# Kernel optimization log

Measured on AMD Instinct MI355X. Metric: run time of the kernel, lower is better.

## Reference

```python
import jax, jax.numpy as jnp
import numpy as np

N = 10000   # num nodes
E = 640000  # num edges
D_IN, D_HID, D_OUT = 128, 256, 128


def _cheb_layer(x, src, dst, dis, W0, W1, b):
    """PyG ChebConv with K=2, sym norm, lambda_max=2.0 (no edge weights):
    out = x @ W0 + (L_hat x) @ W1 + b, with L_hat = -D^{-1/2} A D^{-1/2}."""
    norm = -(dis[src] * dis[dst])                       # [E]
    msg = norm[:, None] * x[src]                        # [E, d]
    tx1 = jax.ops.segment_sum(msg, dst, num_segments=N)  # [N, d]
    return x @ W0 + tx1 @ W1 + b


def setup_inputs() -> dict:
    key = jax.random.key(0)
    ks = jax.random.split(key, 10)

    def glorot(k, fan_in, fan_out):
        s = jnp.sqrt(6.0 / (fan_in + fan_out))
        return jax.random.uniform(k, (fan_in, fan_out), jnp.float32, -s, s)

    x = jax.random.normal(ks[0], (N, D_IN), jnp.float32)
    edge_index = jax.random.randint(ks[1], (2, E), 0, N, jnp.int64)
    edge_type = jax.random.randint(ks[2], (E,), 0, 5, jnp.int64)
    return {
        "x": x,
        "edge_index": edge_index,
        "edge_type": edge_type,
        "W01": glorot(ks[3], D_IN, D_HID),
        "W11": glorot(ks[4], D_IN, D_HID),
        "b1": jnp.zeros((D_HID,), jnp.float32),
        "W02": glorot(ks[5], D_HID, D_HID),
        "W12": glorot(ks[6], D_HID, D_HID),
        "b2": jnp.zeros((D_HID,), jnp.float32),
        "W03": glorot(ks[7], D_HID, D_OUT),
        "W13": glorot(ks[8], D_HID, D_OUT),
        "b3": jnp.zeros((D_OUT,), jnp.float32),
    }


def reference(x, edge_index, edge_type, W01, W11, b1, W02, W12, b2, W03, W13, b3):
    # edge_type is unused by ChebConv (matches the original forward signature).
    src, dst = edge_index[0], edge_index[1]
    deg = jax.ops.segment_sum(jnp.ones((E,), x.dtype), src, num_segments=N)
    dis = jnp.where(deg > 0, jax.lax.rsqrt(jnp.maximum(deg, 1.0)), 0.0)
    # eval mode: dropout(p=0.4) is identity
    h = jax.nn.relu(_cheb_layer(x, src, dst, dis, W01, W11, b1))
    h = jax.nn.relu(_cheb_layer(h, src, dst, dis, W02, W12, b2))
    return _cheb_layer(h, src, dst, dis, W03, W13, b3)
```

## Files before the change

### kernel.cpp

```cpp
#include <hip/hip_runtime.h>

#define D_IN 128
#define D_HID 256
#define D_OUT 128
#define NBIN 10240
#define HB 256

typedef __attribute__((ext_vector_type(8))) unsigned short ushort8v;
typedef __attribute__((ext_vector_type(4))) unsigned short ushort4v;
typedef __attribute__((ext_vector_type(8))) short short8v;
typedef __attribute__((ext_vector_type(4))) float f32x4;

__device__ __forceinline__ unsigned short f2bf(float f) {
    unsigned u = __float_as_uint(f);
    unsigned r = (u + 0x7fffu + ((u >> 16) & 1u)) >> 16;
    return (unsigned short)r;
}
__device__ __forceinline__ float bf2f(unsigned short b) {
    return __uint_as_float((unsigned)b << 16);
}


struct WtrArgs {
    const float* W[6];
    unsigned short* T[6];
    int K[6];
    int N[6];
    const float* xin;
    unsigned short* xout;
    int nElem;
};


__global__ __launch_bounds__(256) void k_hist(const int* __restrict__ src, const int* __restrict__ dst,
                                              unsigned short* __restrict__ psrc,
                                              unsigned short* __restrict__ pdst,
                                              int E, int EPB, WtrArgs wa) {
    __shared__ int h[NBIN];
    int b = blockIdx.x, t = threadIdx.x;
    if (blockIdx.y == 2) {
        const int starts[7] = {0, 32, 64, 128, 192, 224, 256};
        int m = 0;
        while (b >= starts[m + 1]) ++m;
        int local = b - starts[m];
        int K = wa.K[m], N = wa.N[m];
        int kt = K / 32;
        int k0 = (local % kt) * 32, n0 = (local / kt) * 32;
        float (*tile)[33] = (float(*)[33])h;
        int tx = t & 31, ty = t >> 5;
        const float* W = wa.W[m];
        unsigned short* Wt = wa.T[m];
        for (int i = ty; i < 32; i += 8) tile[i][tx] = W[(size_t)(k0 + i) * N + n0 + tx];
        __syncthreads();
        for (int i = ty; i < 32; i += 8) Wt[(size_t)(n0 + i) * K + k0 + tx] = f2bf(tile[tx][i]);
        int stride = HB * 256 * 4;
        for (int i = (b * 256 + t) * 4; i < wa.nElem; i += stride) {
            float4 v = *reinterpret_cast<const float4*>(&wa.xin[i]);
            ushort4v o;
            o[0] = f2bf(v.x); o[1] = f2bf(v.y); o[2] = f2bf(v.z); o[3] = f2bf(v.w);
            *reinterpret_cast<ushort4v*>(&wa.xout[i]) = o;
        }
        return;
    }
    const int* arr = blockIdx.y ? dst : src;
    unsigned short* outp = blockIdx.y ? pdst : psrc;
    for (int i = t; i < NBIN; i += 256) h[i] = 0;
    __syncthreads();
    int beg = b * EPB, end = beg + EPB; if (end > E) end = E;
    for (int e = beg + t; e < end; e += 256)
        atomicAdd(&h[arr[e]], 1);
    __syncthreads();
    for (int i = t; i < NBIN; i += 256)
        outp[(size_t)b * NBIN + i] = (unsigned short)h[i];
}


__global__ __launch_bounds__(256) void k_colsum(const unsigned short* __restrict__ psrc,
                                                unsigned short* __restrict__ pdst,
                                                float* __restrict__ dis, int* __restrict__ cnt) {
    int bin = blockIdx.x * 256 + threadIdx.x;
    if (bin >= NBIN) return;
    int degs = 0;
    for (int b = 0; b < HB; ++b) degs += psrc[(size_t)b * NBIN + bin];
    int c = 0;
    for (int b = 0; b < HB; ++b) {
        int v = pdst[(size_t)b * NBIN + bin];
        pdst[(size_t)b * NBIN + bin] = (unsigned short)c;
        c += v;
    }
    dis[bin] = degs > 0 ? rsqrtf((float)degs) : 0.f;
    cnt[bin] = c;
}


__global__ void k_scan(const int* __restrict__ cnt, int* __restrict__ off, int n, int E) {
    __shared__ int sums[256];
    int t = threadIdx.x;
    int chunk = (n + 255) / 256;
    int beg = t * chunk;
    int end = beg + chunk; if (end > n) end = n;
    int s = 0;
    for (int i = beg; i < end; ++i) s += cnt[i];
    sums[t] = s;
    __syncthreads();
    if (t == 0) {
        int running = 0;
        for (int i = 0; i < 256; ++i) { int tmp = sums[i]; sums[i] = running; running += tmp; }
        off[n] = E;
    }
    __syncthreads();
    int pre = sums[t];
    for (int i = beg; i < end; ++i) { off[i] = pre; pre += cnt[i]; }
}


__global__ __launch_bounds__(256) void k_scatter2(const int* __restrict__ src, const int* __restrict__ dst,
                                                  const float* __restrict__ dis, const int* __restrict__ off,
                                                  const unsigned short* __restrict__ pfx,
                                                  unsigned* __restrict__ edges, int E, int EPB) {
    __shared__ int lcnt[NBIN];
    int b = blockIdx.x, t = threadIdx.x;
    for (int i = t; i < NBIN; i += 256) lcnt[i] = 0;
    __syncthreads();
    int beg = b * EPB, end = beg + EPB; if (end > E) end = E;
    const unsigned short* pf = pfx + (size_t)b * NBIN;
    for (int e = beg + t; e < end; e += 256) {
        int s = src[e], d = dst[e];
        int r = atomicAdd(&lcnt[d], 1);
        int pos = off[d] + (int)pf[d] + r;
        float nv = -(dis[s] * dis[d]);
        edges[pos] = ((unsigned)s << 16) | (unsigned)f2bf(nv);
    }
}


#define AGG_GATHER(eSet, vSet)                                                        \
    _Pragma("unroll")                                                                 \
    for (int u = 0; u < 8; ++u)                                                       \
        vSet[u] = *reinterpret_cast<const ushort8v*>(&xb[(size_t)(eSet[u] >> 16) * D + cbase]);

#define AGG_ACCUM(eSet, vSet)                                                         \
    _Pragma("unroll")                                                                 \
    for (int u = 0; u < 8; ++u) {                                                     \
        float nv = __uint_as_float(eSet[u] << 16);                                    \
        _Pragma("unroll")                                                             \
        for (int j = 0; j < 8; ++j)                                                   \
            acc[j] += nv * bf2f(vSet[u][j]);                                          \
    }

template<int D, bool STBF, bool STF32, bool ADDB>
__global__ __launch_bounds__(256) void k_agg_bf(const int* __restrict__ off,
                                                const unsigned* __restrict__ edges,
                                                const unsigned short* __restrict__ xb,
                                                unsigned short* __restrict__ outb,
                                                float* __restrict__ outf,
                                                const float* __restrict__ base, int n) {
    const int CHUNK = 128;
    const int TPN = CHUNK / 8;
    const int NPB = 256 / TPN;
    int tid = threadIdx.x;
    int node = blockIdx.x * NPB + tid / TPN;
    if (node >= n) return;
    int cbase = blockIdx.y * CHUNK + (tid % TPN) * 8;
    int i = off[node], end = off[node + 1];
    float acc[8] = {};
    int nb = (end - i) >> 3;

    if (nb > 0) {
        unsigned e0[8], e1[8];
        ushort8v v0[8], v1[8];
        #pragma unroll
        for (int u = 0; u < 8; ++u) e0[u] = edges[i + u];
        AGG_GATHER(e0, v0)
        int b = 1;
        for (; b + 1 < nb; b += 2) {
            int base1 = i + b * 8;
            #pragma unroll
            for (int u = 0; u < 8; ++u) e1[u] = edges[base1 + u];
            AGG_GATHER(e1, v1)
            AGG_ACCUM(e0, v0)
            int base0 = i + (b + 1) * 8;
            #pragma unroll
            for (int u = 0; u < 8; ++u) e0[u] = edges[base0 + u];
            AGG_GATHER(e0, v0)
            AGG_ACCUM(e1, v1)
        }
        if (b < nb) {
            int base1 = i + b * 8;
            #pragma unroll
            for (int u = 0; u < 8; ++u) e1[u] = edges[base1 + u];
            AGG_GATHER(e1, v1)
            AGG_ACCUM(e0, v0)
            AGG_ACCUM(e1, v1)
        } else {
            AGG_ACCUM(e0, v0)
        }
    }
    for (int t = i + nb * 8; t < end; ++t) {
        unsigned e = edges[t];
        float nv = __uint_as_float(e << 16);
        ushort8v v = *reinterpret_cast<const ushort8v*>(&xb[(size_t)(e >> 16) * D + cbase]);
        #pragma unroll
        for (int j = 0; j < 8; ++j)
            acc[j] += nv * bf2f(v[j]);
    }

    if (ADDB) {
        float4 b0 = *reinterpret_cast<const float4*>(&base[(size_t)node * D + cbase]);
        float4 b1 = *reinterpret_cast<const float4*>(&base[(size_t)node * D + cbase + 4]);
        acc[0] += b0.x; acc[1] += b0.y; acc[2] += b0.z; acc[3] += b0.w;
        acc[4] += b1.x; acc[5] += b1.y; acc[6] += b1.z; acc[7] += b1.w;
    }
    if (STBF) {
        ushort8v ob;
        #pragma unroll
        for (int j = 0; j < 8; ++j) ob[j] = f2bf(acc[j]);
        *reinterpret_cast<ushort8v*>(&outb[(size_t)node * D + cbase]) = ob;
    }
    if (STF32) {
        float4 o0, o1;
        o0.x = acc[0]; o0.y = acc[1]; o0.z = acc[2]; o0.w = acc[3];
        o1.x = acc[4]; o1.y = acc[5]; o1.z = acc[6]; o1.w = acc[7];
        *reinterpret_cast<float4*>(&outf[(size_t)node * D + cbase]) = o0;
        *reinterpret_cast<float4*>(&outf[(size_t)node * D + cbase + 4]) = o1;
    }
}


#define LDT 72

template<int K, bool RELU, bool HAS_B2, bool HAS_BIAS, bool ST_BF, bool ST_F32>
__global__ __launch_bounds__(256) void k_gemm_mfma(
        const unsigned short* __restrict__ A1, const unsigned short* __restrict__ W0t,
        const unsigned short* __restrict__ A2, const unsigned short* __restrict__ W1t,
        const float* __restrict__ bias,
        float* __restrict__ C, unsigned short* __restrict__ Cb, int M, int N) {
    __shared__ unsigned short As[64 * LDT];
    __shared__ unsigned short Bs[128 * LDT];
    int tid = threadIdx.x, lane = tid & 63, wave = tid >> 6;
    int wm = wave >> 1, wn = wave & 1;
    int row0 = blockIdx.x * 64, col0 = blockIdx.y * 128;
    f32x4 acc[2][4];
    #pragma unroll
    for (int i = 0; i < 2; ++i)
        #pragma unroll
        for (int j = 0; j < 4; ++j)
            acc[i][j] = (f32x4){0.f, 0.f, 0.f, 0.f};

    int aRow = wm * 32 + (lane & 15);
    int bRow = wn * 64 + (lane & 15);
    int kOff = (lane >> 4) * 8;
    int sr = tid >> 2, sc = (tid & 3) * 8;
    int gra = row0 + sr; if (gra >= M) gra = M - 1;

    const int npass = HAS_B2 ? 2 : 1;
    for (int pass = 0; pass < npass; ++pass) {
        const unsigned short* A = pass ? A2 : A1;
        const unsigned short* W = pass ? W1t : W0t;
        for (int k0 = 0; k0 < K; k0 += 64) {
            #pragma unroll
            for (int h = 0; h < 2; ++h) {
                ushort8v va = *reinterpret_cast<const ushort8v*>(&A[(size_t)gra * K + k0 + sc + h * 32]);
                *reinterpret_cast<ushort8v*>(&As[sr * LDT + sc + h * 32]) = va;
            }
            #pragma unroll
            for (int g = 0; g < 2; ++g)
                #pragma unroll
                for (int h = 0; h < 2; ++h) {
                    int r = sr + g * 64;
                    ushort8v vb = *reinterpret_cast<const ushort8v*>(&W[(size_t)(col0 + r) * K + k0 + sc + h * 32]);
                    *reinterpret_cast<ushort8v*>(&Bs[r * LDT + sc + h * 32]) = vb;
                }
            __syncthreads();
            #pragma unroll
            for (int kk = 0; kk < 2; ++kk) {
                int ko = kOff + kk * 32;
                short8v a[2], bb[4];
                #pragma unroll
                for (int i = 0; i < 2; ++i)
                    a[i] = *reinterpret_cast<const short8v*>(&As[(aRow + i * 16) * LDT + ko]);
                #pragma unroll
                for (int i = 0; i < 4; ++i)
                    bb[i] = *reinterpret_cast<const short8v*>(&Bs[(bRow + i * 16) * LDT + ko]);
                #pragma unroll
                for (int mi = 0; mi < 2; ++mi)
                    #pragma unroll
                    for (int ni = 0; ni < 4; ++ni)
                        acc[mi][ni] = __builtin_amdgcn_mfma_f32_16x16x32_bf16(a[mi], bb[ni], acc[mi][ni], 0, 0, 0);
            }
            __syncthreads();
        }
    }

    int colBase = col0 + wn * 64 + (lane & 15);
    int rowSub = (lane >> 4) * 4;
    #pragma unroll
    for (int mi = 0; mi < 2; ++mi) {
        int rowF = row0 + wm * 32 + mi * 16 + rowSub;
        #pragma unroll
        for (int r = 0; r < 4; ++r) {
            int gr = rowF + r;
            if (gr < M) {
                #pragma unroll
                for (int ni = 0; ni < 4; ++ni) {
                    int gc = colBase + ni * 16;
                    float v = acc[mi][ni][r];
                    if (HAS_BIAS) v += bias[gc];
                    if (RELU)     v = fmaxf(v, 0.f);
                    if (ST_F32)   C[(size_t)gr * N + gc] = v;
                    if (ST_BF)    Cb[(size_t)gr * N + gc] = f2bf(v);
                }
            }
        }
    }
}


template<int K>
__global__ __launch_bounds__(256) void k_gemm_dual(
        const unsigned short* __restrict__ A1, const unsigned short* __restrict__ W03t,
        const unsigned short* __restrict__ W13t, const float* __restrict__ bias,
        float* __restrict__ part, unsigned short* __restrict__ y3b, int M) {
    const int N = 128;
    __shared__ unsigned short As[64 * LDT];
    __shared__ unsigned short Bs[128 * LDT];
    int tid = threadIdx.x, lane = tid & 63, wave = tid >> 6;
    int wm = wave >> 1, wn = wave & 1;
    int row0 = blockIdx.x * 64;
    const unsigned short* W = blockIdx.y ? W13t : W03t;
    f32x4 acc[2][4];
    #pragma unroll
    for (int i = 0; i < 2; ++i)
        #pragma unroll
        for (int j = 0; j < 4; ++j)
            acc[i][j] = (f32x4){0.f, 0.f, 0.f, 0.f};

    int aRow = wm * 32 + (lane & 15);
    int bRow = wn * 64 + (lane & 15);
    int kOff = (lane >> 4) * 8;
    int sr = tid >> 2, sc = (tid & 3) * 8;
    int gra = row0 + sr; if (gra >= M) gra = M - 1;

    for (int k0 = 0; k0 < K; k0 += 64) {
        #pragma unroll
        for (int h = 0; h < 2; ++h) {
            ushort8v va = *reinterpret_cast<const ushort8v*>(&A1[(size_t)gra * K + k0 + sc + h * 32]);
            *reinterpret_cast<ushort8v*>(&As[sr * LDT + sc + h * 32]) = va;
        }
        #pragma unroll
        for (int g = 0; g < 2; ++g)
            #pragma unroll
            for (int h = 0; h < 2; ++h) {
                int r = sr + g * 64;
                ushort8v vb = *reinterpret_cast<const ushort8v*>(&W[(size_t)r * K + k0 + sc + h * 32]);
                *reinterpret_cast<ushort8v*>(&Bs[r * LDT + sc + h * 32]) = vb;
            }
        __syncthreads();
        #pragma unroll
        for (int kk = 0; kk < 2; ++kk) {
            int ko = kOff + kk * 32;
            short8v a[2], bb[4];
            #pragma unroll
            for (int i = 0; i < 2; ++i)
                a[i] = *reinterpret_cast<const short8v*>(&As[(aRow + i * 16) * LDT + ko]);
            #pragma unroll
            for (int i = 0; i < 4; ++i)
                bb[i] = *reinterpret_cast<const short8v*>(&Bs[(bRow + i * 16) * LDT + ko]);
            #pragma unroll
            for (int mi = 0; mi < 2; ++mi)
                #pragma unroll
                for (int ni = 0; ni < 4; ++ni)
                    acc[mi][ni] = __builtin_amdgcn_mfma_f32_16x16x32_bf16(a[mi], bb[ni], acc[mi][ni], 0, 0, 0);
        }
        __syncthreads();
    }

    int colBase = wn * 64 + (lane & 15);
    int rowSub = (lane >> 4) * 4;
    bool isPart = (blockIdx.y == 0);
    #pragma unroll
    for (int mi = 0; mi < 2; ++mi) {
        int rowF = row0 + wm * 32 + mi * 16 + rowSub;
        #pragma unroll
        for (int r = 0; r < 4; ++r) {
            int gr = rowF + r;
            if (gr < M) {
                #pragma unroll
                for (int ni = 0; ni < 4; ++ni) {
                    int gc = colBase + ni * 16;
                    float v = acc[mi][ni][r];
                    if (isPart) part[(size_t)gr * N + gc] = v + bias[gc];
                    else        y3b[(size_t)gr * N + gc] = f2bf(v);
                }
            }
        }
    }
}


extern "C" void kernel_launch(void* const* d_in, const int* in_sizes, int n_in,
                              void* d_out, int out_size, void* d_ws, size_t ws_size,
                              hipStream_t stream) {
    const float* x   = (const float*)d_in[0];
    const int*   ei  = (const int*)d_in[1];
    const float* W01 = (const float*)d_in[3];
    const float* W11 = (const float*)d_in[4];
    const float* b1  = (const float*)d_in[5];
    const float* W02 = (const float*)d_in[6];
    const float* W12 = (const float*)d_in[7];
    const float* b2  = (const float*)d_in[8];
    const float* W03 = (const float*)d_in[9];
    const float* W13 = (const float*)d_in[10];
    const float* b3  = (const float*)d_in[11];
    float* out = (float*)d_out;

    const int n = in_sizes[0] / D_IN;
    const int E = in_sizes[1] / 2;
    const int* src = ei;
    const int* dst = ei + E;
    const int EPB = (E + HB - 1) / HB;

    char* wsb = (char*)d_ws;
    float* dis   = (float*)wsb;                   wsb += NBIN * 4;
    int*   cnt   = (int*)wsb;                     wsb += NBIN * 4;
    int*   off   = (int*)wsb;                     wsb += (NBIN + 16) * 4;
    unsigned short* psrc = (unsigned short*)wsb;  wsb += (size_t)HB * NBIN * 2;
    unsigned short* pdst = (unsigned short*)wsb;  wsb += (size_t)HB * NBIN * 2;
    unsigned* edges = (unsigned*)wsb;             wsb += (size_t)E * 4;
    unsigned short* txb  = (unsigned short*)wsb;  wsb += (size_t)n * D_HID * 2;
    float*          part = (float*)wsb;           wsb += (size_t)n * D_OUT * 4;
    unsigned short* x_bf = (unsigned short*)wsb;  wsb += (size_t)n * D_IN * 2;
    unsigned short* h1_bf = (unsigned short*)wsb; wsb += (size_t)n * D_HID * 2;
    unsigned short* h2_bf = (unsigned short*)wsb; wsb += (size_t)n * D_HID * 2;
    unsigned short* y3_bf = (unsigned short*)wsb; wsb += (size_t)n * D_OUT * 2;
    unsigned short* W01t = (unsigned short*)wsb;  wsb += (size_t)D_IN  * D_HID * 2;
    unsigned short* W11t = (unsigned short*)wsb;  wsb += (size_t)D_IN  * D_HID * 2;
    unsigned short* W02t = (unsigned short*)wsb;  wsb += (size_t)D_HID * D_HID * 2;
    unsigned short* W12t = (unsigned short*)wsb;  wsb += (size_t)D_HID * D_HID * 2;
    unsigned short* W03t = (unsigned short*)wsb;  wsb += (size_t)D_HID * D_OUT * 2;
    unsigned short* W13t = (unsigned short*)wsb;  wsb += (size_t)D_HID * D_OUT * 2;

    const int gmx = (n + 63) / 64;
    const int gax = (n + 15) / 16;

    WtrArgs wa;
    wa.W[0] = W01; wa.T[0] = W01t; wa.K[0] = D_IN;  wa.N[0] = D_HID;
    wa.W[1] = W11; wa.T[1] = W11t; wa.K[1] = D_IN;  wa.N[1] = D_HID;
    wa.W[2] = W02; wa.T[2] = W02t; wa.K[2] = D_HID; wa.N[2] = D_HID;
    wa.W[3] = W12; wa.T[3] = W12t; wa.K[3] = D_HID; wa.N[3] = D_HID;
    wa.W[4] = W03; wa.T[4] = W03t; wa.K[4] = D_HID; wa.N[4] = D_OUT;
    wa.W[5] = W13; wa.T[5] = W13t; wa.K[5] = D_HID; wa.N[5] = D_OUT;
    wa.xin = x; wa.xout = x_bf; wa.nElem = n * D_IN;

    k_hist<<<dim3(HB, 3), 256, 0, stream>>>(src, dst, psrc, pdst, E, EPB, wa);
    k_colsum<<<NBIN / 256, 256, 0, stream>>>(psrc, pdst, dis, cnt);
    k_scan<<<1, 256, 0, stream>>>(cnt, off, n, E);
    k_scatter2<<<HB, 256, 0, stream>>>(src, dst, dis, off, pdst, edges, E, EPB);

    k_agg_bf<D_IN, true, false, false><<<dim3(gax, 1), 256, 0, stream>>>(
        off, edges, x_bf, txb, nullptr, nullptr, n);
    k_gemm_mfma<D_IN, true, true, true, true, false><<<dim3(gmx, D_HID / 128), 256, 0, stream>>>(
        x_bf, W01t, txb, W11t, b1, nullptr, h1_bf, n, D_HID);

    k_agg_bf<D_HID, true, false, false><<<dim3(gax, 2), 256, 0, stream>>>(
        off, edges, h1_bf, txb, nullptr, nullptr, n);
    k_gemm_mfma<D_HID, true, true, true, true, false><<<dim3(gmx, D_HID / 128), 256, 0, stream>>>(
        h1_bf, W02t, txb, W12t, b2, nullptr, h2_bf, n, D_HID);

    k_gemm_dual<D_HID><<<dim3(gmx, 2), 256, 0, stream>>>(
        h2_bf, W03t, W13t, b3, part, y3_bf, n);
    k_agg_bf<D_OUT, false, true, true><<<dim3(gax, 1), 256, 0, stream>>>(
        off, edges, y3_bf, nullptr, out, part, n);
}
```

Measured before the change: 162.8 us.

## Gather neighbor features in FP8 for all three sparse aggregations

Adds FP8 copies of the input features, the layer-1 activations and the layer-3 projected features, written by the producer kernels. The aggregation kernels then gather these instead of bf16, halving the bytes per random neighbor row read. Each thread now covers 16 columns of the full row, so the column-split grid dimension goes away. The cost is FP8 quantization error in the aggregated features plus extra FP8 stores in the producers, which may hurt accuracy.

```diff
diff --git a/kernel.cpp b/kernel.cpp
--- a/kernel.cpp
+++ b/kernel.cpp
@@ -10,6 +10,8 @@
 typedef __attribute__((ext_vector_type(4))) unsigned short ushort4v;
 typedef __attribute__((ext_vector_type(8))) short short8v;
 typedef __attribute__((ext_vector_type(4))) float f32x4;
+typedef __attribute__((ext_vector_type(2))) float f32x2;
+typedef __attribute__((ext_vector_type(4))) unsigned int uint4v;
 
 __device__ __forceinline__ unsigned short f2bf(float f) {
     unsigned u = __float_as_uint(f);
@@ -18,6 +20,14 @@
 }
 __device__ __forceinline__ float bf2f(unsigned short b) {
     return __uint_as_float((unsigned)b << 16);
+}
+__device__ __forceinline__ unsigned pk_f8x4(float a, float b, float c, float d) {
+    int v = __builtin_amdgcn_cvt_pk_fp8_f32(a, b, 0, false);
+    v = __builtin_amdgcn_cvt_pk_fp8_f32(c, d, v, true);
+    return (unsigned)v;
+}
+__device__ __forceinline__ unsigned char f8_1(float a) {
+    return (unsigned char)(__builtin_amdgcn_cvt_pk_fp8_f32(a, a, 0, false) & 0xff);
 }
 
 
@@ -28,6 +38,7 @@
     int N[6];
     const float* xin;
     unsigned short* xout;
+    unsigned char* xoutf8;
     int nElem;
 };
 
@@ -59,6 +70,7 @@
             ushort4v o;
             o[0] = f2bf(v.x); o[1] = f2bf(v.y); o[2] = f2bf(v.z); o[3] = f2bf(v.w);
             *reinterpret_cast<ushort4v*>(&wa.xout[i]) = o;
+            *reinterpret_cast<unsigned*>(&wa.xoutf8[i]) = pk_f8x4(v.x, v.y, v.z, v.w);
         }
         return;
     }
@@ -137,38 +149,54 @@
 #define AGG_GATHER(eSet, vSet)                                                        \
     _Pragma("unroll")                                                                 \
     for (int u = 0; u < 8; ++u)                                                       \
-        vSet[u] = *reinterpret_cast<const ushort8v*>(&xb[(size_t)(eSet[u] >> 16) * D + cbase]);
+        vSet[u] = *reinterpret_cast<const uint4v*>(&xf8[(size_t)(eSet[u] >> 16) * D + cbase]);
 
 #define AGG_ACCUM(eSet, vSet)                                                         \
     _Pragma("unroll")                                                                 \
     for (int u = 0; u < 8; ++u) {                                                     \
         float nv = __uint_as_float(eSet[u] << 16);                                    \
         _Pragma("unroll")                                                             \
-        for (int j = 0; j < 8; ++j)                                                   \
-            acc[j] += nv * bf2f(vSet[u][j]);                                          \
+        for (int d = 0; d < 4; ++d) {                                                 \
+            f32x2 lo = __builtin_amdgcn_cvt_pk_f32_fp8((int)vSet[u][d], false);       \
+            f32x2 hi = __builtin_amdgcn_cvt_pk_f32_fp8((int)vSet[u][d], true);        \
+            acc[4*d+0] += nv * lo[0]; acc[4*d+1] += nv * lo[1];                       \
+            acc[4*d+2] += nv * hi[0]; acc[4*d+3] += nv * hi[1];                       \
+        }                                                                             \
+    }
+
+#define AGG_ONE(e)                                                                    \
+    {                                                                                 \
+        float nv = __uint_as_float((e) << 16);                                        \
+        uint4v v = *reinterpret_cast<const uint4v*>(&xf8[(size_t)((e) >> 16) * D + cbase]); \
+        _Pragma("unroll")                                                             \
+        for (int d = 0; d < 4; ++d) {                                                 \
+            f32x2 lo = __builtin_amdgcn_cvt_pk_f32_fp8((int)v[d], false);             \
+            f32x2 hi = __builtin_amdgcn_cvt_pk_f32_fp8((int)v[d], true);              \
+            acc[4*d+0] += nv * lo[0]; acc[4*d+1] += nv * lo[1];                       \
+            acc[4*d+2] += nv * hi[0]; acc[4*d+3] += nv * hi[1];                       \
+        }                                                                             \
     }
 
 template<int D, bool STBF, bool STF32, bool ADDB>
-__global__ __launch_bounds__(256) void k_agg_bf(const int* __restrict__ off,
+__global__ __launch_bounds__(256) void k_agg_f8(const int* __restrict__ off,
                                                 const unsigned* __restrict__ edges,
-                                                const unsigned short* __restrict__ xb,
+                                                const unsigned char* __restrict__ xf8,
                                                 unsigned short* __restrict__ outb,
                                                 float* __restrict__ outf,
                                                 const float* __restrict__ base, int n) {
-    const int CHUNK = 128;
-    const int TPN = CHUNK / 8;
+    const int TPN = D / 16;
     const int NPB = 256 / TPN;
     int tid = threadIdx.x;
     int node = blockIdx.x * NPB + tid / TPN;
     if (node >= n) return;
-    int cbase = blockIdx.y * CHUNK + (tid % TPN) * 8;
+    int cbase = (tid % TPN) * 16;
     int i = off[node], end = off[node + 1];
-    float acc[8] = {};
+    float acc[16] = {};
     int nb = (end - i) >> 3;
 
     if (nb > 0) {
         unsigned e0[8], e1[8];
-        ushort8v v0[8], v1[8];
+        uint4v v0[8], v1[8];
         #pragma unroll
         for (int u = 0; u < 8; ++u) e0[u] = edges[i + u];
         AGG_GATHER(e0, v0)
@@ -198,43 +226,42 @@
     }
     for (int t = i + nb * 8; t < end; ++t) {
         unsigned e = edges[t];
-        float nv = __uint_as_float(e << 16);
-        ushort8v v = *reinterpret_cast<const ushort8v*>(&xb[(size_t)(e >> 16) * D + cbase]);
-        #pragma unroll
-        for (int j = 0; j < 8; ++j)
-            acc[j] += nv * bf2f(v[j]);
+        AGG_ONE(e)
     }
 
     if (ADDB) {
-        float4 b0 = *reinterpret_cast<const float4*>(&base[(size_t)node * D + cbase]);
-        float4 b1 = *reinterpret_cast<const float4*>(&base[(size_t)node * D + cbase + 4]);
-        acc[0] += b0.x; acc[1] += b0.y; acc[2] += b0.z; acc[3] += b0.w;
-        acc[4] += b1.x; acc[5] += b1.y; acc[6] += b1.z; acc[7] += b1.w;
+        #pragma unroll
+        for (int q = 0; q < 4; ++q) {
+            float4 bq = *reinterpret_cast<const float4*>(&base[(size_t)node * D + cbase + q * 4]);
+            acc[q*4+0] += bq.x; acc[q*4+1] += bq.y; acc[q*4+2] += bq.z; acc[q*4+3] += bq.w;
+        }
     }
     if (STBF) {
-        ushort8v ob;
-        #pragma unroll
-        for (int j = 0; j < 8; ++j) ob[j] = f2bf(acc[j]);
-        *reinterpret_cast<ushort8v*>(&outb[(size_t)node * D + cbase]) = ob;
+        ushort8v ob0, ob1;
+        #pragma unroll
+        for (int j = 0; j < 8; ++j) { ob0[j] = f2bf(acc[j]); ob1[j] = f2bf(acc[8 + j]); }
+        *reinterpret_cast<ushort8v*>(&outb[(size_t)node * D + cbase]) = ob0;
+        *reinterpret_cast<ushort8v*>(&outb[(size_t)node * D + cbase + 8]) = ob1;
     }
     if (STF32) {
-        float4 o0, o1;
-        o0.x = acc[0]; o0.y = acc[1]; o0.z = acc[2]; o0.w = acc[3];
-        o1.x = acc[4]; o1.y = acc[5]; o1.z = acc[6]; o1.w = acc[7];
-        *reinterpret_cast<float4*>(&outf[(size_t)node * D + cbase]) = o0;
-        *reinterpret_cast<float4*>(&outf[(size_t)node * D + cbase + 4]) = o1;
+        #pragma unroll
+        for (int q = 0; q < 4; ++q) {
+            float4 o;
+            o.x = acc[q*4+0]; o.y = acc[q*4+1]; o.z = acc[q*4+2]; o.w = acc[q*4+3];
+            *reinterpret_cast<float4*>(&outf[(size_t)node * D + cbase + q * 4]) = o;
+        }
     }
 }
 
 
 #define LDT 72
 
-template<int K, bool RELU, bool HAS_B2, bool HAS_BIAS, bool ST_BF, bool ST_F32>
+template<int K, bool RELU, bool HAS_B2, bool HAS_BIAS, bool ST_BF, bool ST_F8>
 __global__ __launch_bounds__(256) void k_gemm_mfma(
         const unsigned short* __restrict__ A1, const unsigned short* __restrict__ W0t,
         const unsigned short* __restrict__ A2, const unsigned short* __restrict__ W1t,
         const float* __restrict__ bias,
-        float* __restrict__ C, unsigned short* __restrict__ Cb, int M, int N) {
+        unsigned short* __restrict__ Cb, unsigned char* __restrict__ Cf8, int M, int N) {
     __shared__ unsigned short As[64 * LDT];
     __shared__ unsigned short Bs[128 * LDT];
     int tid = threadIdx.x, lane = tid & 63, wave = tid >> 6;
@@ -307,8 +334,8 @@
                     float v = acc[mi][ni][r];
                     if (HAS_BIAS) v += bias[gc];
                     if (RELU)     v = fmaxf(v, 0.f);
-                    if (ST_F32)   C[(size_t)gr * N + gc] = v;
                     if (ST_BF)    Cb[(size_t)gr * N + gc] = f2bf(v);
+                    if (ST_F8)    Cf8[(size_t)gr * N + gc] = f8_1(v);
                 }
             }
         }
@@ -320,7 +347,7 @@
 __global__ __launch_bounds__(256) void k_gemm_dual(
         const unsigned short* __restrict__ A1, const unsigned short* __restrict__ W03t,
         const unsigned short* __restrict__ W13t, const float* __restrict__ bias,
-        float* __restrict__ part, unsigned short* __restrict__ y3b, int M) {
+        float* __restrict__ part, unsigned char* __restrict__ y3f8, int M) {
     const int N = 128;
     __shared__ unsigned short As[64 * LDT];
     __shared__ unsigned short Bs[128 * LDT];
@@ -390,7 +417,7 @@
                     int gc = colBase + ni * 16;
                     float v = acc[mi][ni][r];
                     if (isPart) part[(size_t)gr * N + gc] = v + bias[gc];
-                    else        y3b[(size_t)gr * N + gc] = f2bf(v);
+                    else        y3f8[(size_t)gr * N + gc] = f8_1(v);
                 }
             }
         }
@@ -432,7 +459,10 @@
     unsigned short* x_bf = (unsigned short*)wsb;  wsb += (size_t)n * D_IN * 2;
     unsigned short* h1_bf = (unsigned short*)wsb; wsb += (size_t)n * D_HID * 2;
     unsigned short* h2_bf = (unsigned short*)wsb; wsb += (size_t)n * D_HID * 2;
-    unsigned short* y3_bf = (unsigned short*)wsb; wsb += (size_t)n * D_OUT * 2;
+    unsigned char* x_f8  = (unsigned char*)wsb;   wsb += (size_t)n * D_IN;
+    unsigned char* h1_f8 = (unsigned char*)wsb;   wsb += (size_t)n * D_HID;
+    unsigned char* y3_f8 = (unsigned char*)wsb;   wsb += (size_t)n * D_OUT;
+    wsb = (char*)(((size_t)wsb + 255) & ~(size_t)255);
     unsigned short* W01t = (unsigned short*)wsb;  wsb += (size_t)D_IN  * D_HID * 2;
     unsigned short* W11t = (unsigned short*)wsb;  wsb += (size_t)D_IN  * D_HID * 2;
     unsigned short* W02t = (unsigned short*)wsb;  wsb += (size_t)D_HID * D_HID * 2;
@@ -441,7 +471,8 @@
     unsigned short* W13t = (unsigned short*)wsb;  wsb += (size_t)D_HID * D_OUT * 2;
 
     const int gmx = (n + 63) / 64;
-    const int gax = (n + 15) / 16;
+    const int ga128 = (n + 31) / 32;
+    const int ga256 = (n + 15) / 16;
 
     WtrArgs wa;
     wa.W[0] = W01; wa.T[0] = W01t; wa.K[0] = D_IN;  wa.N[0] = D_HID;
@@ -450,25 +481,25 @@
     wa.W[3] = W12; wa.T[3] = W12t; wa.K[3] = D_HID; wa.N[3] = D_HID;
     wa.W[4] = W03; wa.T[4] = W03t; wa.K[4] = D_HID; wa.N[4] = D_OUT;
     wa.W[5] = W13; wa.T[5] = W13t; wa.K[5] = D_HID; wa.N[5] = D_OUT;
-    wa.xin = x; wa.xout = x_bf; wa.nElem = n * D_IN;
+    wa.xin = x; wa.xout = x_bf; wa.xoutf8 = x_f8; wa.nElem = n * D_IN;
 
     k_hist<<<dim3(HB, 3), 256, 0, stream>>>(src, dst, psrc, pdst, E, EPB, wa);
     k_colsum<<<NBIN / 256, 256, 0, stream>>>(psrc, pdst, dis, cnt);
     k_scan<<<1, 256, 0, stream>>>(cnt, off, n, E);
     k_scatter2<<<HB, 256, 0, stream>>>(src, dst, dis, off, pdst, edges, E, EPB);
 
-    k_agg_bf<D_IN, true, false, false><<<dim3(gax, 1), 256, 0, stream>>>(
-        off, edges, x_bf, txb, nullptr, nullptr, n);
-    k_gemm_mfma<D_IN, true, true, true, true, false><<<dim3(gmx, D_HID / 128), 256, 0, stream>>>(
-        x_bf, W01t, txb, W11t, b1, nullptr, h1_bf, n, D_HID);
-
-    k_agg_bf<D_HID, true, false, false><<<dim3(gax, 2), 256, 0, stream>>>(
-        off, edges, h1_bf, txb, nullptr, nullptr, n);
+    k_agg_f8<D_IN, true, false, false><<<ga128, 256, 0, stream>>>(
+        off, edges, x_f8, txb, nullptr, nullptr, n);
+    k_gemm_mfma<D_IN, true, true, true, true, true><<<dim3(gmx, D_HID / 128), 256, 0, stream>>>(
+        x_bf, W01t, txb, W11t, b1, h1_bf, h1_f8, n, D_HID);
+
+    k_agg_f8<D_HID, true, false, false><<<ga256, 256, 0, stream>>>(
+        off, edges, h1_f8, txb, nullptr, nullptr, n);
     k_gemm_mfma<D_HID, true, true, true, true, false><<<dim3(gmx, D_HID / 128), 256, 0, stream>>>(
-        h1_bf, W02t, txb, W12t, b2, nullptr, h2_bf, n, D_HID);
+        h1_bf, W02t, txb, W12t, b2, h2_bf, nullptr, n, D_HID);
 
     k_gemm_dual<D_HID><<<dim3(gmx, 2), 256, 0, stream>>>(
-        h2_bf, W03t, W13t, b3, part, y3_bf, n);
-    k_agg_bf<D_OUT, false, true, true><<<dim3(gax, 1), 256, 0, stream>>>(
-        off, edges, y3_bf, nullptr, out, part, n);
-}
+        h2_bf, W03t, W13t, b3, part, y3_f8, n);
+    k_agg_f8<D_OUT, false, true, true><<<ga128, 256, 0, stream>>>(
+        off, edges, y3_f8, nullptr, out, part, n);
+}
```

New measurement: 155.5 us. 1.05x faster.
